# Kernel tuning notes

Hardware: AMD Instinct MI355X
Metric: run time of the kernel (lower is better)

Reference implementation:

```python
import jax, jax.numpy as jnp
import numpy as np

TAU_M = 0.01
TAU_I = 0.005
DT = 0.001
ALPHA = float(np.exp(-DT / TAU_M))  # applied to current (as in source)
BETA = float(np.exp(-DT / TAU_I))   # applied to voltage (as in source)

B, T, N, NI = 16, 1000, 4096, 1024


def setup_inputs() -> dict:
    key = jax.random.key(0)
    k0, k1, k2, k3 = jax.random.split(key, 4)
    neuron_types = jnp.where(jax.random.uniform(k0, (N,)) < 0.8, 1, -1).astype(jnp.int32)
    recurrent_weights = (jax.random.normal(k1, (N, N), jnp.float32) / np.sqrt(N)).astype(jnp.float32)
    feedforward_weights = (jax.random.normal(k2, (N, NI), jnp.float32) / np.sqrt(NI)).astype(jnp.float32)
    inputs = (jax.random.uniform(k3, (B, T, NI)) < 0.05).astype(jnp.float32)
    return {
        "initial_v": jnp.zeros((B, N), jnp.float32),
        "initial_I": jnp.zeros((B, N), jnp.float32),
        "inputs": inputs,
        "recurrent_weights": recurrent_weights,
        "feedforward_weights": feedforward_weights,
        "E_weight": jnp.asarray(1.0, jnp.float32),
        "I_weight": jnp.asarray(1.0, jnp.float32),
        "E_v_th": jnp.asarray(1.0, jnp.float32),
        "I_v_th": jnp.asarray(1.0, jnp.float32),
        "neuron_types": neuron_types,
        "n_steps": T,
    }


def reference(initial_v, initial_I, inputs, recurrent_weights, feedforward_weights,
              E_weight, I_weight, E_v_th, I_v_th, neuron_types, n_steps):
    exc = neuron_types == 1
    # per-column scaling, exactly as source: W * scale[None, :]
    scaled_w = recurrent_weights * jnp.where(exc, E_weight, I_weight)[None, :]  # (N, N)
    v_th = jnp.where(exc, E_v_th, I_v_th)  # (N,)
    # precomputed feedforward drive, as in source: (B, T, N)
    ff = jnp.einsum("bti,ni->btn", inputs, feedforward_weights)
    # NOTE: source initializes s = zeros and never updates it in the loop,
    # so the recurrent term s @ scaled_w is identically zero. Replicated faithfully.
    s = jnp.zeros_like(initial_v)  # (B, N)

    def step(carry, ff_t):
        v, cur = carry
        cur = ALPHA * cur + ff_t + s @ scaled_w
        v = BETA * v + cur - s
        spikes = (v >= v_th[None, :]).astype(v.dtype)
        v = v * (1.0 - spikes)
        return (v, cur), None

    (v, cur), _ = jax.lax.scan(step, (initial_v, initial_I), jnp.swapaxes(ff, 0, 1))
    return (v, cur)
```

## Files before the change

kernel.cpp:

```cpp
#include <hip/hip_runtime.h>
#include <cmath>
#include <cstdint>
#include <cstddef>


typedef _Float16 half8 __attribute__((ext_vector_type(8)));
typedef float floatx4 __attribute__((ext_vector_type(4)));

#define WSCALE 1024.0f
#define WSCALE_INV (1.0f / 1024.0f)

#define VMW4 asm volatile("s_waitcnt vmcnt(4)" ::: "memory")
#define VMW0 asm volatile("s_waitcnt vmcnt(0)" ::: "memory")
#define BAR  __builtin_amdgcn_s_barrier()

__device__ __forceinline__ void gload16(const void* g, void* l) {
    __builtin_amdgcn_global_load_lds(
        (const __attribute__((address_space(1))) unsigned int*)g,
        (__attribute__((address_space(3))) unsigned int*)l, 16, 0, 0);
}

__global__ __launch_bounds__(256) void k_wprep(const float* __restrict__ Wff,
                                               _Float16* __restrict__ Wt2,
                                               int N, int NI) {
    int tid = blockIdx.x * 256 + (int)threadIdx.x;
    int per_row = NI >> 3;
    int n = tid / per_row;
    int ic = (tid - n * per_row) << 3;
    if (n >= N) return;
    const float4* src = (const float4*)(Wff + (size_t)n * NI + ic);
    float4 w0 = src[0], w1 = src[1];
    float wv[8] = {w0.x, w0.y, w0.z, w0.w, w1.x, w1.y, w1.z, w1.w};
    half8 hi, lo;
#pragma unroll
    for (int j = 0; j < 8; ++j) {
        float w = wv[j] * WSCALE;
        _Float16 h = (_Float16)w;
        hi[j] = h;
        lo[j] = (_Float16)(w - (float)h);
    }
    *(half8*)(Wt2 + (size_t)n * (2 * NI) + ic) = hi;
    *(half8*)(Wt2 + (size_t)n * (2 * NI) + NI + ic) = lo;
}

__device__ __forceinline__ void xconv_range(const float* __restrict__ x,
                                            _Float16* __restrict__ X16,
                                            int g0, int gstep, int xrows,
                                            int t0, int tc, int T, int NI) {
    int per_row = NI >> 3;
    int G = xrows * per_row;
    for (int g = g0; g < G; g += gstep) {
        int r = g / per_row;
        int gi = g - r * per_row;
        int b = r / tc;
        int tl = r - b * tc;
        size_t off = ((size_t)(b * T + t0 + tl) * NI) + ((size_t)gi << 3);
        const float4* src = (const float4*)(x + off);
        float4 a = src[0], c = src[1];
        half8 o;
        o[0] = (_Float16)a.x; o[1] = (_Float16)a.y;
        o[2] = (_Float16)a.z; o[3] = (_Float16)a.w;
        o[4] = (_Float16)c.x; o[5] = (_Float16)c.y;
        o[6] = (_Float16)c.z; o[7] = (_Float16)c.w;
        *(half8*)(X16 + off) = o;
    }
}

__global__ __launch_bounds__(256) void k_xpre(const float* __restrict__ x,
                                              _Float16* __restrict__ X16,
                                              int xrows, int t0, int tc,
                                              int T, int NI) {
    xconv_range(x, X16, blockIdx.x * 256 + (int)threadIdx.x,
                (int)gridDim.x * 256, xrows, t0, tc, T, NI);
}

__global__ __launch_bounds__(512, 2) void k_chunk(
    const _Float16* __restrict__ Wt2, const _Float16* __restrict__ X16,
    _Float16* __restrict__ x16w, const float* __restrict__ xin,
    float* __restrict__ ff_dst, const float* __restrict__ ff_src,
    const float* __restrict__ vin, const float* __restrict__ cin,
    float* __restrict__ vout, float* __restrict__ cout,
    const int* __restrict__ ntype, const float* __restrict__ Evth_p,
    const float* __restrict__ Ivth_p,
    int T, int tc_ff, int t0_ff, int tc_rec, int N, int NI,
    float alpha, float beta, int nff, int nrec, int mv,
    int xrows, int t0_x, int tc_x)
{
    __shared__ _Float16 smA[2][2][256 * 32];
    __shared__ _Float16 smB[2][2][256 * 32];
    int blk = blockIdx.x;
    int tid = (int)threadIdx.x;
    if (blk < nff) {
        int Ntiles = N >> 8;
        int mt = blk / Ntiles;
        int nt = blk - mt * Ntiles;
        int m0 = mt << 8, n0 = nt << 8;
        int wid = tid >> 6, lane = tid & 63;
        int wr = wid >> 2, wc = wid & 3;
        int ln15 = lane & 15, kh = lane >> 4;

        int slot4 = (lane & 3) ^ ((lane >> 3) & 3);
        const char* srcA[2]; const char* srcB[2];
        int dB0 = (wid * 2) * 512;
        int dB1 = dB0 + 512;
#pragma unroll
        for (int q = 0; q < 2; ++q) {
            int rl = (wid * 2 + q) * 16 + (lane >> 2);
            int rA = m0 + rl;
            if (rA > mv - 1) rA = mv - 1;
            int b = rA / tc_ff;
            int tl = rA - b * tc_ff;
            srcA[q] = (const char*)(X16 + (size_t)(b * T + t0_ff + tl) * NI + slot4 * 8);
            srcB[q] = (const char*)(Wt2 + (size_t)(n0 + rl) * (2 * NI) + slot4 * 8);
        }
        int amask = NI - 1;

#define STAGE_A(S2, KS, KOFS) { \
        gload16(srcA[0] + (KOFS), &smA[S2][KS][dB0]); \
        gload16(srcA[1] + (KOFS), &smA[S2][KS][dB1]); }
#define STAGE_B(S2, KS, KOFS) { \
        gload16(srcB[0] + (KOFS), &smB[S2][KS][dB0]); \
        gload16(srcB[1] + (KOFS), &smB[S2][KS][dB1]); }

        STAGE_A(0, 0, 0);
        STAGE_B(0, 0, 0);
        STAGE_A(0, 1, 64);
        STAGE_B(0, 1, 64);
        VMW4; BAR;

        int sa  = ((kh ^ ((ln15 >> 1) & 3)) << 3);
        int aro = (wr * 128 + ln15) * 32 + sa;
        int bro = (wc * 64 + ln15) * 32 + sa;

        floatx4 acc[8][4] = {};
        int NKT = (2 * NI) >> 6;

        for (int kt = 0; kt < NKT; ++kt) {
            int s = kt & 1, s2 = s ^ 1;
            bool pre = (kt + 1 < NKT);
            int j64 = (kt + 1) << 6;
            int kA0 = ((j64) & amask) * 2;
            int kA1 = ((j64 + 32) & amask) * 2;
            int kB0 = j64 * 2;
            int kB1 = (j64 + 32) * 2;
            half8 a[4], b[4];
#pragma unroll
            for (int f = 0; f < 4; ++f) b[f] = *(const half8*)(&smB[s][0][bro + f * 512]);
#pragma unroll
            for (int f = 0; f < 4; ++f) a[f] = *(const half8*)(&smA[s][0][aro + f * 512]);
            if (pre) STAGE_A(s2, 0, kA0);
            BAR;
            __builtin_amdgcn_s_setprio(1);
#pragma unroll
            for (int fi = 0; fi < 4; ++fi)
#pragma unroll
                for (int fj = 0; fj < 4; ++fj)
                    acc[fi][fj] = __builtin_amdgcn_mfma_f32_16x16x32_f16(a[fi], b[fj], acc[fi][fj], 0, 0, 0);
            __builtin_amdgcn_s_setprio(0);
            BAR;
#pragma unroll
            for (int f = 0; f < 4; ++f) a[f] = *(const half8*)(&smA[s][0][aro + 2048 + f * 512]);
            if (pre) { STAGE_B(s2, 0, kB0); VMW4; } else { VMW0; }
            BAR;
            __builtin_amdgcn_s_setprio(1);
#pragma unroll
            for (int fi = 0; fi < 4; ++fi)
#pragma unroll
                for (int fj = 0; fj < 4; ++fj)
                    acc[4 + fi][fj] = __builtin_amdgcn_mfma_f32_16x16x32_f16(a[fi], b[fj], acc[4 + fi][fj], 0, 0, 0);
            __builtin_amdgcn_s_setprio(0);
            BAR;
#pragma unroll
            for (int f = 0; f < 4; ++f) b[f] = *(const half8*)(&smB[s][1][bro + f * 512]);
#pragma unroll
            for (int f = 0; f < 4; ++f) a[f] = *(const half8*)(&smA[s][1][aro + f * 512]);
            if (pre) STAGE_A(s2, 1, kA1);
            BAR;
            __builtin_amdgcn_s_setprio(1);
#pragma unroll
            for (int fi = 0; fi < 4; ++fi)
#pragma unroll
                for (int fj = 0; fj < 4; ++fj)
                    acc[fi][fj] = __builtin_amdgcn_mfma_f32_16x16x32_f16(a[fi], b[fj], acc[fi][fj], 0, 0, 0);
            __builtin_amdgcn_s_setprio(0);
            BAR;
#pragma unroll
            for (int f = 0; f < 4; ++f) a[f] = *(const half8*)(&smA[s][1][aro + 2048 + f * 512]);
            if (pre) { STAGE_B(s2, 1, kB1); VMW4; }
            BAR;
            __builtin_amdgcn_s_setprio(1);
#pragma unroll
            for (int fi = 0; fi < 4; ++fi)
#pragma unroll
                for (int fj = 0; fj < 4; ++fj)
                    acc[4 + fi][fj] = __builtin_amdgcn_mfma_f32_16x16x32_f16(a[fi], b[fj], acc[4 + fi][fj], 0, 0, 0);
            __builtin_amdgcn_s_setprio(0);
            BAR;
        }
#undef STAGE_A
#undef STAGE_B
#pragma unroll
        for (int ai = 0; ai < 8; ++ai) {
            int r0 = m0 + wr * 128 + (ai >> 2) * 64 + (ai & 3) * 16 + kh * 4;
#pragma unroll
            for (int fj = 0; fj < 4; ++fj) {
                int nn = n0 + wc * 64 + fj * 16 + ln15;
                float* p = ff_dst + (size_t)r0 * N + nn;
#pragma unroll
                for (int e = 0; e < 4; ++e)
                    if (r0 + e < mv) p[(size_t)e * N] = acc[ai][fj][e] * WSCALE_INV;
            }
        }
    } else if (blk < nff + nrec) {
        int r = (blk - nff) * 512 + tid;
        int e0 = r << 2;
        int b = e0 / N;
        int n = e0 - b * N;
        float vth[4], v[4], cu[4];
#pragma unroll
        for (int j = 0; j < 4; ++j) vth[j] = (ntype[n + j] == 1) ? Evth_p[0] : Ivth_p[0];
        {
            float4 a0 = *(const float4*)(vin + e0);
            float4 b0 = *(const float4*)(cin + e0);
            v[0]=a0.x; v[1]=a0.y; v[2]=a0.z; v[3]=a0.w;
            cu[0]=b0.x; cu[1]=b0.y; cu[2]=b0.z; cu[3]=b0.w;
        }
        const float* f = ff_src + (size_t)b * tc_rec * N + n;

#define ST1(J, X) \
        cu[J] = __fadd_rn(__fmul_rn(alpha, cu[J]), (X)); \
        v[J]  = __fadd_rn(__fmul_rn(beta, v[J]), cu[J]); \
        v[J]  = (v[J] >= vth[J]) ? 0.0f : v[J];
#define STEP4(A) { ST1(0, (A).x) ST1(1, (A).y) ST1(2, (A).z) ST1(3, (A).w) }

        int t = 0;
        if (tc_rec >= 16) {
            float4 X[8], Y[8];
#pragma unroll
            for (int k = 0; k < 8; ++k) X[k] = *(const float4*)(f + (size_t)k * N);
            for (t = 0; t + 16 <= tc_rec; t += 8) {
#pragma unroll
                for (int k = 0; k < 8; ++k) Y[k] = *(const float4*)(f + (size_t)(t + 8 + k) * N);
#pragma unroll
                for (int k = 0; k < 8; ++k) { STEP4(X[k]) }
#pragma unroll
                for (int k = 0; k < 8; ++k) X[k] = Y[k];
            }
#pragma unroll
            for (int k = 0; k < 8; ++k) { STEP4(X[k]) }
            t += 8;
        }
        for (; t < tc_rec; ++t) {
            float4 a = *(const float4*)(f + (size_t)t * N);
            STEP4(a)
        }
#undef STEP4
#undef ST1
        {
            float4 o0 = {v[0], v[1], v[2], v[3]};
            float4 o1 = {cu[0], cu[1], cu[2], cu[3]};
            *(float4*)(vout + e0) = o0;
            *(float4*)(cout + e0) = o1;
        }
    } else {
        int xb = blk - nff - nrec;
        int nxb = (int)gridDim.x - nff - nrec;
        xconv_range(xin, x16w, xb * 512 + tid, nxb * 512,
                    xrows, t0_x, tc_x, T, NI);
    }
}

extern "C" void kernel_launch(void* const* d_in, const int* in_sizes, int n_in,
                              void* d_out, int out_size, void* d_ws, size_t ws_size,
                              hipStream_t stream) {
    const float* initial_v = (const float*)d_in[0];
    const float* initial_I = (const float*)d_in[1];
    const float* inputs    = (const float*)d_in[2];
    const float* Wff       = (const float*)d_in[4];
    const float* Evth      = (const float*)d_in[7];
    const float* Ivth      = (const float*)d_in[8];
    const int*   ntype     = (const int*)d_in[9];

    const int N  = in_sizes[9];
    const int B  = in_sizes[0] / N;
    const int NI = in_sizes[4] / N;
    const int T  = in_sizes[2] / (B * NI);

    char* ws = (char*)d_ws;
    _Float16* Wt2 = (_Float16*)ws;
    size_t wt_b  = (size_t)N * 2 * NI * sizeof(_Float16);
    _Float16* X16 = (_Float16*)(ws + wt_b);
    size_t x_b   = (size_t)B * T * NI * sizeof(_Float16);
    float* state = (float*)(ws + wt_b + x_b);
    size_t st_b  = (size_t)2 * B * N * sizeof(float);
    char*  ffbase = ws + wt_b + x_b + st_b;
    size_t fixed  = wt_b + x_b + st_b;

    size_t avail = (ws_size > fixed) ? (ws_size - fixed) : 0;
    size_t per_t = (size_t)B * N * sizeof(float);
    int TC = (int)(avail / (2 * per_t));
    if (TC > 208) TC = 208;
    if (TC > T) TC = T;
    TC &= ~15;
    if (TC < 16) TC = 16;

    float* fbuf[2];
    fbuf[0] = (float*)ffbase;
    fbuf[1] = (float*)(ffbase + (size_t)TC * per_t);

    const float alpha = (float)exp(-0.001 / 0.01);
    const float beta  = (float)exp(-0.001 / 0.005);

    float* st_v = state;
    float* st_c = state + (size_t)B * N;

    static const int MAXCH = 1024;
    int t0s[MAXCH], tcs[MAXCH];
    int nch = 0;
    {
        int t0 = 0;
        while (t0 < T && nch < MAXCH) {
            int tc = T - t0;
            if (tc > TC) tc = TC;
            t0s[nch] = t0; tcs[nch] = tc;
            t0 += tc; ++nch;
        }
    }

    k_wprep<<<dim3((N * NI / 8 + 255) / 256), 256, 0, stream>>>(Wff, Wt2, N, NI);
    k_xpre<<<dim3(384), 256, 0, stream>>>(inputs, X16, B * tcs[0], 0, tcs[0], T, NI);

    for (int k = 0; k <= nch; ++k) {
        int tc_ff  = (k < nch) ? tcs[k] : 0;
        int t0_ff  = (k < nch) ? t0s[k] : 0;
        int tc_rec = (k >= 1) ? tcs[k - 1] : 0;
        int nrec   = (k >= 1) ? (B * N) / (512 * 4) : 0;
        int tc_x   = (k + 1 < nch) ? tcs[k + 1] : 0;
        int t0_x   = (k + 1 < nch) ? t0s[k + 1] : 0;
        int nxb    = (tc_x > 0) ? 16 : 0;
        float* ffd = fbuf[k & 1];
        const float* ffs = fbuf[(k ^ 1) & 1];
        const float* vi = (k == 1) ? initial_v : st_v;
        const float* ci = (k == 1) ? initial_I : st_c;
        float* vo = (k == nch) ? (float*)d_out : st_v;
        float* co = (k == nch) ? ((float*)d_out + (size_t)B * N) : st_c;
        int mv  = B * tc_ff;
        int nff = (tc_ff > 0) ? (((mv + 255) >> 8) * (N >> 8)) : 0;
        int grid = nff + nrec + nxb;
        if (grid == 0) continue;
        k_chunk<<<dim3(grid), 512, 0, stream>>>(Wt2, X16, X16, inputs, ffd, ffs,
                                                vi, ci, vo, co,
                                                ntype, Evth, Ivth,
                                                T, tc_ff, t0_ff, tc_rec, N, NI,
                                                alpha, beta, nff, nrec, mv,
                                                B * tc_x, t0_x, tc_x);
    }
}
```

Before: 476.6 us.

## Replace double-buffered GEMM loop with triple-buffered single-barrier pipeline

Restructures the feedforward GEMM main loop from a two-stage double buffer with four barriers per 64-wide K step into a three-stage ring of 32-wide K slabs. Each iteration waits on global-to-LDS loads and takes one barrier, prefetches two steps ahead, then runs 32 MFMAs. This cuts barrier count and keeps more loads in flight. It drops the s_setprio hints, and since the LDS footprint is 3/4 of before, occupancy may also change.

```diff
diff --git a/kernel.cpp b/kernel.cpp
--- a/kernel.cpp
+++ b/kernel.cpp
@@ -86,8 +86,8 @@
     float alpha, float beta, int nff, int nrec, int mv,
     int xrows, int t0_x, int tc_x)
 {
-    __shared__ _Float16 smA[2][2][256 * 32];
-    __shared__ _Float16 smB[2][2][256 * 32];
+    __shared__ _Float16 smA[3][256 * 32];
+    __shared__ _Float16 smB[3][256 * 32];
     int blk = blockIdx.x;
     int tid = (int)threadIdx.x;
     if (blk < nff) {
@@ -115,90 +115,51 @@
         }
         int amask = NI - 1;
 
-#define STAGE_A(S2, KS, KOFS) { \
-        gload16(srcA[0] + (KOFS), &smA[S2][KS][dB0]); \
-        gload16(srcA[1] + (KOFS), &smA[S2][KS][dB1]); }
-#define STAGE_B(S2, KS, KOFS) { \
-        gload16(srcB[0] + (KOFS), &smB[S2][KS][dB0]); \
-        gload16(srcB[1] + (KOFS), &smB[S2][KS][dB1]); }
-
-        STAGE_A(0, 0, 0);
-        STAGE_B(0, 0, 0);
-        STAGE_A(0, 1, 64);
-        STAGE_B(0, 1, 64);
-        VMW4; BAR;
+#define STAGE(S, KOFA, KOFB) { \
+        gload16(srcA[0] + (KOFA), &smA[S][dB0]); \
+        gload16(srcA[1] + (KOFA), &smA[S][dB1]); \
+        gload16(srcB[0] + (KOFB), &smB[S][dB0]); \
+        gload16(srcB[1] + (KOFB), &smB[S][dB1]); }
+
+        STAGE(0, 0, 0);
+        STAGE(1, 64, 64);
 
         int sa  = ((kh ^ ((ln15 >> 1) & 3)) << 3);
         int aro = (wr * 128 + ln15) * 32 + sa;
         int bro = (wc * 64 + ln15) * 32 + sa;
 
         floatx4 acc[8][4] = {};
-        int NKT = (2 * NI) >> 6;
+        int NKT = (2 * NI) >> 5;
+        int s = 0;
 
         for (int kt = 0; kt < NKT; ++kt) {
-            int s = kt & 1, s2 = s ^ 1;
-            bool pre = (kt + 1 < NKT);
-            int j64 = (kt + 1) << 6;
-            int kA0 = ((j64) & amask) * 2;
-            int kA1 = ((j64 + 32) & amask) * 2;
-            int kB0 = j64 * 2;
-            int kB1 = (j64 + 32) * 2;
-            half8 a[4], b[4];
-#pragma unroll
-            for (int f = 0; f < 4; ++f) b[f] = *(const half8*)(&smB[s][0][bro + f * 512]);
-#pragma unroll
-            for (int f = 0; f < 4; ++f) a[f] = *(const half8*)(&smA[s][0][aro + f * 512]);
-            if (pre) STAGE_A(s2, 0, kA0);
+            if (kt + 1 < NKT) { VMW4; } else { VMW0; }
             BAR;
-            __builtin_amdgcn_s_setprio(1);
+            if (kt + 2 < NKT) {
+                int s2 = s + 2; if (s2 >= 3) s2 -= 3;
+                int j32 = (kt + 2) << 5;
+                STAGE(s2, ((j32) & amask) * 2, j32 * 2);
+            }
+            half8 a0[4], a1[4], b0[4];
+#pragma unroll
+            for (int f = 0; f < 4; ++f) b0[f] = *(const half8*)(&smB[s][bro + f * 512]);
+#pragma unroll
+            for (int f = 0; f < 4; ++f) a0[f] = *(const half8*)(&smA[s][aro + f * 512]);
+#pragma unroll
+            for (int f = 0; f < 4; ++f) a1[f] = *(const half8*)(&smA[s][aro + 2048 + f * 512]);
 #pragma unroll
             for (int fi = 0; fi < 4; ++fi)
 #pragma unroll
                 for (int fj = 0; fj < 4; ++fj)
-                    acc[fi][fj] = __builtin_amdgcn_mfma_f32_16x16x32_f16(a[fi], b[fj], acc[fi][fj], 0, 0, 0);
-            __builtin_amdgcn_s_setprio(0);
-            BAR;
-#pragma unroll
-            for (int f = 0; f < 4; ++f) a[f] = *(const half8*)(&smA[s][0][aro + 2048 + f * 512]);
-            if (pre) { STAGE_B(s2, 0, kB0); VMW4; } else { VMW0; }
-            BAR;
-            __builtin_amdgcn_s_setprio(1);
+                    acc[fi][fj] = __builtin_amdgcn_mfma_f32_16x16x32_f16(a0[fi], b0[fj], acc[fi][fj], 0, 0, 0);
 #pragma unroll
             for (int fi = 0; fi < 4; ++fi)
 #pragma unroll
                 for (int fj = 0; fj < 4; ++fj)
-                    acc[4 + fi][fj] = __builtin_amdgcn_mfma_f32_16x16x32_f16(a[fi], b[fj], acc[4 + fi][fj], 0, 0, 0);
-            __builtin_amdgcn_s_setprio(0);
-            BAR;
-#pragma unroll
-            for (int f = 0; f < 4; ++f) b[f] = *(const half8*)(&smB[s][1][bro + f * 512]);
-#pragma unroll
-            for (int f = 0; f < 4; ++f) a[f] = *(const half8*)(&smA[s][1][aro + f * 512]);
-            if (pre) STAGE_A(s2, 1, kA1);
-            BAR;
-            __builtin_amdgcn_s_setprio(1);
-#pragma unroll
-            for (int fi = 0; fi < 4; ++fi)
-#pragma unroll
-                for (int fj = 0; fj < 4; ++fj)
-                    acc[fi][fj] = __builtin_amdgcn_mfma_f32_16x16x32_f16(a[fi], b[fj], acc[fi][fj], 0, 0, 0);
-            __builtin_amdgcn_s_setprio(0);
-            BAR;
-#pragma unroll
-            for (int f = 0; f < 4; ++f) a[f] = *(const half8*)(&smA[s][1][aro + 2048 + f * 512]);
-            if (pre) { STAGE_B(s2, 1, kB1); VMW4; }
-            BAR;
-            __builtin_amdgcn_s_setprio(1);
-#pragma unroll
-            for (int fi = 0; fi < 4; ++fi)
-#pragma unroll
-                for (int fj = 0; fj < 4; ++fj)
-                    acc[4 + fi][fj] = __builtin_amdgcn_mfma_f32_16x16x32_f16(a[fi], b[fj], acc[4 + fi][fj], 0, 0, 0);
-            __builtin_amdgcn_s_setprio(0);
-            BAR;
-        }
-#undef STAGE_A
-#undef STAGE_B
+                    acc[4 + fi][fj] = __builtin_amdgcn_mfma_f32_16x16x32_f16(a1[fi], b0[fj], acc[4 + fi][fj], 0, 0, 0);
+            ++s; if (s >= 3) s = 0;
+        }
+#undef STAGE
 #pragma unroll
         for (int ai = 0; ai < 8; ++ai) {
             int r0 = m0 + wr * 128 + (ai >> 2) * 64 + (ai & 3) * 16 + kh * 4;
```

Measured after the change: 570.5 us. 19.7% more time.

## Reuse A tile across hi/lo weight halves to halve A loads

Applied to the files above, without the earlier changes.

The FF GEMM uses a split-fp16 weight (hi and lo halves concatenated along K, twice NI), so the same A slice was loaded twice. Each k-step now loads one A tile plus both the hi and lo B tiles for the same K range. The A fragments are kept in registers for both MFMA passes, which cuts A global/LDS traffic and shared memory use. In exchange it raises register pressure (a0, a1, bh, bl held together) and changes the vmcnt wait pattern.

```diff
diff --git a/kernel.cpp b/kernel.cpp
--- a/kernel.cpp
+++ b/kernel.cpp
@@ -11,6 +11,7 @@
 #define WSCALE_INV (1.0f / 1024.0f)
 
 #define VMW4 asm volatile("s_waitcnt vmcnt(4)" ::: "memory")
+#define VMW2 asm volatile("s_waitcnt vmcnt(2)" ::: "memory")
 #define VMW0 asm volatile("s_waitcnt vmcnt(0)" ::: "memory")
 #define BAR  __builtin_amdgcn_s_barrier()
 
@@ -86,8 +87,9 @@
     float alpha, float beta, int nff, int nrec, int mv,
     int xrows, int t0_x, int tc_x)
 {
-    __shared__ _Float16 smA[2][2][256 * 32];
-    __shared__ _Float16 smB[2][2][256 * 32];
+    __shared__ _Float16 smA[2][256 * 32];
+    __shared__ _Float16 smBh[2][256 * 32];
+    __shared__ _Float16 smBl[2][256 * 32];
     int blk = blockIdx.x;
     int tid = (int)threadIdx.x;
     if (blk < nff) {
@@ -113,92 +115,87 @@
             srcA[q] = (const char*)(X16 + (size_t)(b * T + t0_ff + tl) * NI + slot4 * 8);
             srcB[q] = (const char*)(Wt2 + (size_t)(n0 + rl) * (2 * NI) + slot4 * 8);
         }
-        int amask = NI - 1;
-
-#define STAGE_A(S2, KS, KOFS) { \
-        gload16(srcA[0] + (KOFS), &smA[S2][KS][dB0]); \
-        gload16(srcA[1] + (KOFS), &smA[S2][KS][dB1]); }
-#define STAGE_B(S2, KS, KOFS) { \
-        gload16(srcB[0] + (KOFS), &smB[S2][KS][dB0]); \
-        gload16(srcB[1] + (KOFS), &smB[S2][KS][dB1]); }
-
-        STAGE_A(0, 0, 0);
-        STAGE_B(0, 0, 0);
-        STAGE_A(0, 1, 64);
-        STAGE_B(0, 1, 64);
-        VMW4; BAR;
+        int NIb = NI * 2;
+
+#define STAGE_A(S2, KOFS) { \
+        gload16(srcA[0] + (KOFS), &smA[S2][dB0]); \
+        gload16(srcA[1] + (KOFS), &smA[S2][dB1]); }
+#define STAGE_BH(S2, KOFS) { \
+        gload16(srcB[0] + (KOFS), &smBh[S2][dB0]); \
+        gload16(srcB[1] + (KOFS), &smBh[S2][dB1]); }
+#define STAGE_BL(S2, KOFS) { \
+        gload16(srcB[0] + (KOFS), &smBl[S2][dB0]); \
+        gload16(srcB[1] + (KOFS), &smBl[S2][dB1]); }
+
+        STAGE_A(0, 0);
+        STAGE_BH(0, 0);
+        STAGE_BL(0, NIb);
+        VMW2; BAR;
 
         int sa  = ((kh ^ ((ln15 >> 1) & 3)) << 3);
         int aro = (wr * 128 + ln15) * 32 + sa;
         int bro = (wc * 64 + ln15) * 32 + sa;
 
         floatx4 acc[8][4] = {};
-        int NKT = (2 * NI) >> 6;
+        int NKT = NI >> 5;
 
         for (int kt = 0; kt < NKT; ++kt) {
             int s = kt & 1, s2 = s ^ 1;
             bool pre = (kt + 1 < NKT);
-            int j64 = (kt + 1) << 6;
-            int kA0 = ((j64) & amask) * 2;
-            int kA1 = ((j64 + 32) & amask) * 2;
-            int kB0 = j64 * 2;
-            int kB1 = (j64 + 32) * 2;
-            half8 a[4], b[4];
-#pragma unroll
-            for (int f = 0; f < 4; ++f) b[f] = *(const half8*)(&smB[s][0][bro + f * 512]);
-#pragma unroll
-            for (int f = 0; f < 4; ++f) a[f] = *(const half8*)(&smA[s][0][aro + f * 512]);
-            if (pre) STAGE_A(s2, 0, kA0);
+            int j32b = (kt + 1) << 6;
+            half8 a0[4], a1[4], bh[4], bl[4];
+#pragma unroll
+            for (int f = 0; f < 4; ++f) bh[f] = *(const half8*)(&smBh[s][bro + f * 512]);
+#pragma unroll
+            for (int f = 0; f < 4; ++f) a0[f] = *(const half8*)(&smA[s][aro + f * 512]);
+            if (pre) STAGE_A(s2, j32b);
             BAR;
             __builtin_amdgcn_s_setprio(1);
 #pragma unroll
             for (int fi = 0; fi < 4; ++fi)
 #pragma unroll
                 for (int fj = 0; fj < 4; ++fj)
-                    acc[fi][fj] = __builtin_amdgcn_mfma_f32_16x16x32_f16(a[fi], b[fj], acc[fi][fj], 0, 0, 0);
+                    acc[fi][fj] = __builtin_amdgcn_mfma_f32_16x16x32_f16(a0[fi], bh[fj], acc[fi][fj], 0, 0, 0);
             __builtin_amdgcn_s_setprio(0);
             BAR;
 #pragma unroll
-            for (int f = 0; f < 4; ++f) a[f] = *(const half8*)(&smA[s][0][aro + 2048 + f * 512]);
-            if (pre) { STAGE_B(s2, 0, kB0); VMW4; } else { VMW0; }
+            for (int f = 0; f < 4; ++f) a1[f] = *(const half8*)(&smA[s][aro + 2048 + f * 512]);
+            if (pre) { STAGE_BH(s2, j32b); VMW4; } else { VMW0; }
             BAR;
             __builtin_amdgcn_s_setprio(1);
 #pragma unroll
             for (int fi = 0; fi < 4; ++fi)
 #pragma unroll
                 for (int fj = 0; fj < 4; ++fj)
-                    acc[4 + fi][fj] = __builtin_amdgcn_mfma_f32_16x16x32_f16(a[fi], b[fj], acc[4 + fi][fj], 0, 0, 0);
+                    acc[4 + fi][fj] = __builtin_amdgcn_mfma_f32_16x16x32_f16(a1[fi], bh[fj], acc[4 + fi][fj], 0, 0, 0);
             __builtin_amdgcn_s_setprio(0);
             BAR;
 #pragma unroll
-            for (int f = 0; f < 4; ++f) b[f] = *(const half8*)(&smB[s][1][bro + f * 512]);
-#pragma unroll
-            for (int f = 0; f < 4; ++f) a[f] = *(const half8*)(&smA[s][1][aro + f * 512]);
-            if (pre) STAGE_A(s2, 1, kA1);
+            for (int f = 0; f < 4; ++f) bl[f] = *(const half8*)(&smBl[s][bro + f * 512]);
+            if (pre) STAGE_BL(s2, NIb + j32b);
             BAR;
             __builtin_amdgcn_s_setprio(1);
 #pragma unroll
             for (int fi = 0; fi < 4; ++fi)
 #pragma unroll
                 for (int fj = 0; fj < 4; ++fj)
-                    acc[fi][fj] = __builtin_amdgcn_mfma_f32_16x16x32_f16(a[fi], b[fj], acc[fi][fj], 0, 0, 0);
+                    acc[fi][fj] = __builtin_amdgcn_mfma_f32_16x16x32_f16(a0[fi], bl[fj], acc[fi][fj], 0, 0, 0);
             __builtin_amdgcn_s_setprio(0);
             BAR;
-#pragma unroll
-            for (int f = 0; f < 4; ++f) a[f] = *(const half8*)(&smA[s][1][aro + 2048 + f * 512]);
-            if (pre) { STAGE_B(s2, 1, kB1); VMW4; }
+            if (pre) { VMW2; }
             BAR;
             __builtin_amdgcn_s_setprio(1);
 #pragma unroll
             for (int fi = 0; fi < 4; ++fi)
 #pragma unroll
                 for (int fj = 0; fj < 4; ++fj)
-                    acc[4 + fi][fj] = __builtin_amdgcn_mfma_f32_16x16x32_f16(a[fi], b[fj], acc[4 + fi][fj], 0, 0, 0);
+                    acc[4 + fi][fj] = __builtin_amdgcn_mfma_f32_16x16x32_f16(a1[fi], bl[fj], acc[4 + fi][fj], 0, 0, 0);
             __builtin_amdgcn_s_setprio(0);
             BAR;
         }
 #undef STAGE_A
-#undef STAGE_B
+#undef STAGE_BH
+#undef STAGE_BL
 #pragma unroll
         for (int ai = 0; ai < 8; ++ai) {
             int r0 = m0 + wr * 128 + (ai >> 2) * 64 + (ai & 3) * 16 + kh * 4;
```

After: 439.6 us. 7.8% less time.
